# Kernel optimization log

Measured on AMD Instinct MI355X. Metric: run time of the kernel, lower is better.

Reference implementation:

```python
import jax, jax.numpy as jnp
import numpy as np


def setup_inputs() -> dict:
    key = jax.random.key(0)
    k1, k2, k3, k4 = jax.random.split(key, 4)
    B, N, D, L = 4, 512, 256, 64
    x = jax.random.normal(k1, (B, N, D), dtype=jnp.float32)
    adj = jax.random.uniform(k2, (B, N, N), dtype=jnp.float32)
    W_proj = jax.random.normal(k3, (L, D), dtype=jnp.float32) * (1.0 / np.sqrt(D))
    learn_w = jax.random.uniform(k4, (L,), dtype=jnp.float32)  # init.uniform_(0,1)
    return {"x": x, "adj": adj, "W_proj": W_proj, "learn_w": learn_w}


def reference(x, adj, W_proj, learn_w):
    # x: [B,N,D]; projection (no bias): x_hat [B,N,L]
    x_hat = jnp.einsum('bnd,ld->bnl', x, W_proj)
    # pairwise L1-style abs difference: [B,N,N,L]
    diff = jnp.abs(x_hat[:, :, None, :] - x_hat[:, None, :, :])
    # weighted reduce over feature dim: [B,N,N]
    dist = jnp.einsum('bijl,l->bij', diff, learn_w)
    out = jax.nn.leaky_relu(dist, negative_slope=0.01)
    out = out - jnp.max(out, axis=-1, keepdims=True)
    soft_adj = adj * jnp.exp(out)
    # NOTE: faithful to original: epsilon added AFTER the division
    soft_adj = soft_adj / jnp.sum(soft_adj, axis=-1, keepdims=True) + 1e-10
    return soft_adj
```

## Files before the change

kernel.cpp:

```cpp
#include <hip/hip_runtime.h>
#include <math.h>

#define BB 4
#define NN 512
#define DD 256
#define LL 64

#define WST 260
#define IPB 4

__global__ __launch_bounds__(256) void k1_proj(const float* __restrict__ x,
                                               const float* __restrict__ Wp,
                                               const float* __restrict__ lw,
                                               float* __restrict__ xhatT) {
  __shared__ __align__(16) float Wl[32 * WST];
  __shared__ __align__(16) float xs[8 * WST];
  const int bx = blockIdx.x;
  const int nt = bx & 63;
  const int lh = (bx >> 6) & 1;
  const int b  = bx >> 7;
  const int n0 = nt * 8;
  const int t  = threadIdx.x;

  const int ll = t >> 3;
  const int r  = t & 7;

  float wl = lw[lh * 32 + ll];

  const float4* Wp4 = (const float4*)Wp + (size_t)lh * 32 * 64;
  #pragma unroll
  for (int it = 0; it < 8; ++it) {
    int idx = it * 256 + t;
    int lr  = idx >> 6;
    int dq  = idx & 63;
    *(float4*)&Wl[lr * WST + dq * 4] = Wp4[idx];
  }
  {
    const float4* x4 = (const float4*)(x + ((size_t)b * NN + n0) * DD);
    #pragma unroll
    for (int it = 0; it < 2; ++it) {
      int idx = it * 256 + t;
      *(float4*)&xs[(idx >> 6) * WST + (idx & 63) * 4] = x4[idx];
    }
  }
  __syncthreads();

  const float4* wrow = (const float4*)&Wl[ll * WST];
  const float4* xrow = (const float4*)&xs[r * WST];
  float4 a = make_float4(0.f, 0.f, 0.f, 0.f);
  #pragma unroll 8
  for (int dd = 0; dd < 64; ++dd) {
    float4 wv = wrow[dd];
    float4 xv = xrow[dd];
    a.x += xv.x * wv.x;
    a.y += xv.y * wv.y;
    a.z += xv.z * wv.z;
    a.w += xv.w * wv.w;
  }
  xhatT[((size_t)b * LL + lh * 32 + ll) * NN + n0 + r] =
      wl * ((a.x + a.y) + (a.z + a.w));
}

__global__ __launch_bounds__(512, 4) void k2_main(const float* __restrict__ xhatT,
                                                  const float* __restrict__ adj,
                                                  float* __restrict__ out) {
  __shared__ float redm[IPB * 8];
  __shared__ float reds[IPB * 8];

  const int bx   = blockIdx.x;
  const int b    = bx >> 7;
  const int i0   = (bx & 127) * IPB;
  const int t    = threadIdx.x;
  const int wave = t >> 6;
  const int lane = t & 63;

  const float* xb = xhatT + (size_t)b * (LL * NN);

  const float* adjb = adj + ((size_t)b * NN + i0) * NN;
  float adjv[IPB];
  #pragma unroll
  for (int r = 0; r < IPB; ++r) adjv[r] = adjb[(size_t)r * NN + t];

  float acc[IPB] = {0.f, 0.f, 0.f, 0.f};
  #pragma unroll 16
  for (int l = 0; l < LL; ++l) {
    float  p  = xb[l * NN + t];
    float4 xi = *(const float4*)(xb + l * NN + i0);
    acc[0] += fabsf(xi.x - p);
    acc[1] += fabsf(xi.y - p);
    acc[2] += fabsf(xi.z - p);
    acc[3] += fabsf(xi.w - p);
  }

  #pragma unroll
  for (int r = 0; r < IPB; ++r) {
    float d = acc[r];
    acc[r] = d >= 0.f ? d : 0.01f * d;
  }

  #pragma unroll
  for (int r = 0; r < IPB; ++r) {
    float m = acc[r];
    #pragma unroll
    for (int off = 32; off > 0; off >>= 1)
      m = fmaxf(m, __shfl_xor(m, off, 64));
    if (lane == 0) redm[r * 8 + wave] = m;
  }
  __syncthreads();

  float e[IPB];
  #pragma unroll
  for (int r = 0; r < IPB; ++r) {
    float m = redm[r * 8 + 0];
    #pragma unroll
    for (int k = 1; k < 8; ++k) m = fmaxf(m, redm[r * 8 + k]);
    e[r] = adjv[r] * __expf(acc[r] - m);
  }

  #pragma unroll
  for (int r = 0; r < IPB; ++r) {
    float s = e[r];
    #pragma unroll
    for (int off = 32; off > 0; off >>= 1)
      s += __shfl_xor(s, off, 64);
    if (lane == 0) reds[r * 8 + wave] = s;
  }
  __syncthreads();

  float* outb = out + ((size_t)b * NN + i0) * NN;
  #pragma unroll
  for (int r = 0; r < IPB; ++r) {
    float s = reds[r * 8 + 0];
    #pragma unroll
    for (int k = 1; k < 8; ++k) s += reds[r * 8 + k];
    outb[(size_t)r * NN + t] = e[r] / s + 1e-10f;
  }
}

extern "C" void kernel_launch(void* const* d_in, const int* in_sizes, int n_in,
                              void* d_out, int out_size, void* d_ws, size_t ws_size,
                              hipStream_t stream) {
  const float* x   = (const float*)d_in[0];
  const float* adj = (const float*)d_in[1];
  const float* Wp  = (const float*)d_in[2];
  const float* lw  = (const float*)d_in[3];
  float* out   = (float*)d_out;
  float* xhatT = (float*)d_ws;

  hipLaunchKernelGGL(k1_proj, dim3(BB * 2 * (NN / 8)), dim3(256), 0, stream,
                     x, Wp, lw, xhatT);
  hipLaunchKernelGGL(k2_main, dim3(BB * NN / IPB), dim3(512), 0, stream,
                     xhatT, adj, out);
}
```

Baseline: 74.10 us.

## Store projected features in l4-interleaved float4 layout and stage row features in LDS

The projection kernel now writes x_hat in a [B,16,N,4] interleaved layout so the main kernel can load four feature values per column with one float4 load instead of four scalar loads. The per-row (i) features are staged once into shared memory, which replaces the repeated broadcast global loads inside the loop. This adds one extra __syncthreads and changes the k1 store pattern to scattered 4-byte writes with stride 16 bytes, which may coalesce less well.

```diff
diff --git a/kernel.cpp b/kernel.cpp
--- a/kernel.cpp
+++ b/kernel.cpp
@@ -12,7 +12,7 @@
 __global__ __launch_bounds__(256) void k1_proj(const float* __restrict__ x,
                                                const float* __restrict__ Wp,
                                                const float* __restrict__ lw,
-                                               float* __restrict__ xhatT) {
+                                               float* __restrict__ xhat) {
   __shared__ __align__(16) float Wl[32 * WST];
   __shared__ __align__(16) float xs[8 * WST];
   const int bx = blockIdx.x;
@@ -57,13 +57,15 @@
     a.z += xv.z * wv.z;
     a.w += xv.w * wv.w;
   }
-  xhatT[((size_t)b * LL + lh * 32 + ll) * NN + n0 + r] =
+  const int l = lh * 32 + ll;
+  xhat[(((size_t)b * 16 + (l >> 2)) * NN + n0 + r) * 4 + (l & 3)] =
       wl * ((a.x + a.y) + (a.z + a.w));
 }
 
-__global__ __launch_bounds__(512, 4) void k2_main(const float* __restrict__ xhatT,
+__global__ __launch_bounds__(512, 4) void k2_main(const float* __restrict__ xhat,
                                                   const float* __restrict__ adj,
                                                   float* __restrict__ out) {
+  __shared__ __align__(16) float4 xi_s[16 * IPB];
   __shared__ float redm[IPB * 8];
   __shared__ float reds[IPB * 8];
 
@@ -74,22 +76,29 @@
   const int wave = t >> 6;
   const int lane = t & 63;
 
-  const float* xb = xhatT + (size_t)b * (LL * NN);
+  const float4* xb4 = (const float4*)xhat + (size_t)b * 16 * NN;
 
   const float* adjb = adj + ((size_t)b * NN + i0) * NN;
   float adjv[IPB];
   #pragma unroll
   for (int r = 0; r < IPB; ++r) adjv[r] = adjb[(size_t)r * NN + t];
 
+  if (t < 16 * IPB) {
+    int l4 = t >> 2, r = t & 3;
+    xi_s[l4 * IPB + r] = xb4[l4 * NN + i0 + r];
+  }
+  __syncthreads();
+
   float acc[IPB] = {0.f, 0.f, 0.f, 0.f};
-  #pragma unroll 16
-  for (int l = 0; l < LL; ++l) {
-    float  p  = xb[l * NN + t];
-    float4 xi = *(const float4*)(xb + l * NN + i0);
-    acc[0] += fabsf(xi.x - p);
-    acc[1] += fabsf(xi.y - p);
-    acc[2] += fabsf(xi.z - p);
-    acc[3] += fabsf(xi.w - p);
+  #pragma unroll 4
+  for (int l4 = 0; l4 < 16; ++l4) {
+    float4 xj = xb4[l4 * NN + t];
+    #pragma unroll
+    for (int r = 0; r < IPB; ++r) {
+      float4 xi = xi_s[l4 * IPB + r];
+      acc[r] += fabsf(xi.x - xj.x) + fabsf(xi.y - xj.y) +
+                fabsf(xi.z - xj.z) + fabsf(xi.w - xj.w);
+    }
   }
 
   #pragma unroll
@@ -144,11 +153,11 @@
   const float* adj = (const float*)d_in[1];
   const float* Wp  = (const float*)d_in[2];
   const float* lw  = (const float*)d_in[3];
-  float* out   = (float*)d_out;
-  float* xhatT = (float*)d_ws;
+  float* out  = (float*)d_out;
+  float* xhat = (float*)d_ws;
 
   hipLaunchKernelGGL(k1_proj, dim3(BB * 2 * (NN / 8)), dim3(256), 0, stream,
-                     x, Wp, lw, xhatT);
+                     x, Wp, lw, xhat);
   hipLaunchKernelGGL(k2_main, dim3(BB * NN / IPB), dim3(512), 0, stream,
-                     xhatT, adj, out);
+                     xhat, adj, out);
 }
```

Measured after the change: 75.17 us. Within noise of the previous version (+1.5%).
